# Performance work log

Hardware: AMD Instinct MI355X
Metric: run time of the kernel (lower is better)

The kernel has to match this reference:

```python
import jax, jax.numpy as jnp
import numpy as np


def setup_inputs() -> dict:
    key = jax.random.key(0)
    k1, k2 = jax.random.split(key)
    B, C, H, W, T = 64, 128, 8, 8, 100
    outputs = jax.random.normal(k1, (B, C, H, W, T), dtype=jnp.float32)
    target = jax.random.uniform(k2, (B, C, H, W, T), dtype=jnp.float32)
    return {"outputs": outputs, "target": target, "n_steps": T, "tau_s": 2}


def _psp(x, tau_s):
    # x: [B, C, H, W, T]; fixed-coefficient leaky integrator over last axis.
    # syn_t = syn_{t-1} * (1 - 1/tau_s) + x_t ; out_t = syn_t / tau_s
    decay = 1.0 - 1.0 / tau_s
    xt = jnp.moveaxis(x, -1, 0)  # [T, B, C, H, W]

    def step(syn, x_t):
        syn = syn * decay + x_t
        return syn, syn / tau_s

    syn0 = jnp.zeros(x.shape[:-1], dtype=x.dtype)
    _, syns = jax.lax.scan(step, syn0, xt)
    return jnp.moveaxis(syns, 0, -1)  # [B, C, H, W, T]


def reference(outputs, target, n_steps, tau_s):
    # n_steps is implied by the trailing axis; kept for signature fidelity.
    target_psp = _psp(target, float(tau_s))
    delta = outputs - target_psp
    return 0.5 * jnp.sum(delta * delta)
```

## Files before the change

kernel.cpp:

```cpp
#include <hip/hip_runtime.h>


constexpr int T   = 100;
constexpr int SEG = 25;
constexpr int PIX = 16;
constexpr int TF  = PIX * T;
constexpr int NCH = (TF * 4) / 1024;
constexpr int NV4 = TF / 4;

typedef const __attribute__((address_space(1))) void* gas_t;
typedef __attribute__((address_space(3))) void*       las_t;
typedef float f4 __attribute__((ext_vector_type(4)));

__global__ __launch_bounds__(64) void spike_loss_kernel(
    const float* __restrict__ tgt,
    const float* __restrict__ outs,
    const int*   __restrict__ tau_p,
    float*       __restrict__ out,
    int n_tiles, int tiles_per_block)
{
    __shared__ __align__(16) float lds_t[2][TF];

    const float tau     = (float)tau_p[0];
    const float inv_tau = 1.0f / tau;
    const float decay   = 1.0f - inv_tau;
    float d25 = 1.0f;
    #pragma unroll
    for (int i = 0; i < SEG; ++i) d25 *= decay;
    const float d50 = d25 * d25;

    const int tid = threadIdx.x;

    const int first = blockIdx.x * tiles_per_block;
    int cnt = n_tiles - first;
    if (cnt < 0) cnt = 0;
    if (cnt > tiles_per_block) cnt = tiles_per_block;
    if (cnt <= 0) return;

    float acc = 0.0f;

    auto stage = [&](int tile, int buf) {
        const float* gt = tgt + (size_t)tile * TF;
        #pragma unroll
        for (int c = 0; c < NCH; ++c) {
            __builtin_amdgcn_global_load_lds((gas_t)(gt + c * 256 + tid * 4),
                (las_t)&lds_t[buf][c * 256], 16, 0, 0);
        }
        __builtin_amdgcn_global_load_lds((gas_t)(gt + NCH * 256 + tid),
            (las_t)&lds_t[buf][NCH * 256], 4, 0, 0);
    };

    auto process = [&](int buf) {
        const int p    = tid >> 2;
        const int q    = tid & 3;
        const int base = p * T + q * SEG;

        float s[SEG];
        float syn = 0.0f;
        #pragma unroll
        for (int i = 0; i < SEG; ++i) {
            syn = fmaf(syn, decay, lds_t[buf][base + i]);
            s[i] = syn;
        }
        const float f1 = __shfl_up(syn, 1, 64);
        const float f2 = __shfl_up(syn, 2, 64);
        const float f3 = __shfl_up(syn, 3, 64);
        float carry = (q >= 1) ? f1 : 0.0f;
        if (q >= 2) carry = fmaf(f2, d25, carry);
        if (q >= 3) carry = fmaf(f3, d50, carry);

        float cp = carry;
        #pragma unroll
        for (int i = 0; i < SEG; ++i) {
            cp *= decay;
            lds_t[buf][base + i] = s[i] + cp;
        }
    };

    auto pass2 = [&](int tile, int buf) {
        const f4* o4 = (const f4*)(outs + (size_t)tile * TF);
        const f4* p4 = (const f4*)lds_t[buf];
        #pragma unroll
        for (int j = 0; j < NV4 / 64; ++j) {
            const int idx = tid + 64 * j;
            const f4 o = o4[idx];
            const f4 sy = p4[idx];
            #pragma unroll
            for (int c = 0; c < 4; ++c) {
                const float d = fmaf(sy[c], -inv_tau, o[c]);
                acc = fmaf(d, d, acc);
            }
        }
        if (tid < NV4 - (NV4 / 64) * 64) {
            const int idx = (NV4 / 64) * 64 + tid;
            const f4 o = o4[idx];
            const f4 sy = p4[idx];
            #pragma unroll
            for (int c = 0; c < 4; ++c) {
                const float d = fmaf(sy[c], -inv_tau, o[c]);
                acc = fmaf(d, d, acc);
            }
        }
    };

    stage(first, 0);

    for (int k = 0; k < cnt; ++k) {
        if (k + 1 < cnt) {
            stage(first + k + 1, (k + 1) & 1);
            asm volatile("s_waitcnt vmcnt(7)" ::: "memory");
        } else {
            asm volatile("s_waitcnt vmcnt(0)" ::: "memory");
        }
        process(k & 1);
        asm volatile("s_waitcnt lgkmcnt(0)" ::: "memory");
        pass2(first + k, k & 1);
        asm volatile("s_waitcnt lgkmcnt(0)" ::: "memory");
    }

    #pragma unroll
    for (int off = 32; off > 0; off >>= 1)
        acc += __shfl_down(acc, off, 64);
    if (tid == 0)
        atomicAdd(out, 0.5f * acc);
}

extern "C" void kernel_launch(void* const* d_in, const int* in_sizes, int n_in,
                              void* d_out, int out_size, void* d_ws, size_t ws_size,
                              hipStream_t stream) {
    const float* outs = (const float*)d_in[0];
    const float* tgt  = (const float*)d_in[1];
    const int* tau_p  = (const int*)d_in[3];
    float* out        = (float*)d_out;

    const int n_pixels = in_sizes[0] / T;
    const int n_tiles  = n_pixels / PIX;

    const int block = 64;
    const int grid  = 3072;
    const int tiles_per_block = (n_tiles + grid - 1) / grid;

    hipMemsetAsync(out, 0, sizeof(float), stream);

    spike_loss_kernel<<<grid, block, 0, stream>>>(
        tgt, outs, tau_p, out, n_tiles, tiles_per_block);
}
```

Before: 429.0 us.

## Stage outputs via LDS and fuse scan with loss, using 16-byte-aligned segments

The outputs tensor is now prefetched into LDS with async global_load_lds alongside the target, and the loss is computed in the same pass as the carry fix-up. This removes the write-back of the scanned values to LDS and the separate pass that reread them. Each pixel's time axis is split into segments of 28, 28, 28 and 16 so LDS reads can be 16-byte vectors, and the carry constants are recomputed to match. The grid is also halved so each block processes more tiles, and LDS usage doubles, which may lower occupancy.

Measured after the change: 419.2 us. 1.02x faster.

```diff
diff --git a/kernel.cpp b/kernel.cpp
--- a/kernel.cpp
+++ b/kernel.cpp
@@ -2,11 +2,9 @@
 
 
 constexpr int T   = 100;
-constexpr int SEG = 25;
 constexpr int PIX = 16;
 constexpr int TF  = PIX * T;
 constexpr int NCH = (TF * 4) / 1024;
-constexpr int NV4 = TF / 4;
 
 typedef const __attribute__((address_space(1))) void* gas_t;
 typedef __attribute__((address_space(3))) void*       las_t;
@@ -20,14 +18,15 @@
     int n_tiles, int tiles_per_block)
 {
     __shared__ __align__(16) float lds_t[2][TF];
+    __shared__ __align__(16) float lds_o[2][TF];
 
     const float tau     = (float)tau_p[0];
     const float inv_tau = 1.0f / tau;
     const float decay   = 1.0f - inv_tau;
-    float d25 = 1.0f;
+    float d28 = 1.0f;
     #pragma unroll
-    for (int i = 0; i < SEG; ++i) d25 *= decay;
-    const float d50 = d25 * d25;
+    for (int i = 0; i < 28; ++i) d28 *= decay;
+    const float d56 = d28 * d28;
 
     const int tid = threadIdx.x;
 
@@ -40,65 +39,61 @@
     float acc = 0.0f;
 
     auto stage = [&](int tile, int buf) {
-        const float* gt = tgt + (size_t)tile * TF;
+        const float* gt = tgt  + (size_t)tile * TF;
+        const float* go = outs + (size_t)tile * TF;
         #pragma unroll
         for (int c = 0; c < NCH; ++c) {
             __builtin_amdgcn_global_load_lds((gas_t)(gt + c * 256 + tid * 4),
                 (las_t)&lds_t[buf][c * 256], 16, 0, 0);
+            __builtin_amdgcn_global_load_lds((gas_t)(go + c * 256 + tid * 4),
+                (las_t)&lds_o[buf][c * 256], 16, 0, 0);
         }
         __builtin_amdgcn_global_load_lds((gas_t)(gt + NCH * 256 + tid),
             (las_t)&lds_t[buf][NCH * 256], 4, 0, 0);
+        __builtin_amdgcn_global_load_lds((gas_t)(go + NCH * 256 + tid),
+            (las_t)&lds_o[buf][NCH * 256], 4, 0, 0);
     };
 
-    auto process = [&](int buf) {
-        const int p    = tid >> 2;
-        const int q    = tid & 3;
-        const int base = p * T + q * SEG;
+    auto consume = [&](int buf) {
+        const int p  = tid >> 2;
+        const int q  = tid & 3;
+        const int fb = p * T + q * 28;
+        const f4* tb = (const f4*)&lds_t[buf][fb];
+        const f4* ob = (const f4*)&lds_o[buf][fb];
+        const int segn = (q == 3) ? 16 : 28;
 
-        float s[SEG];
+        float s[28];
         float syn = 0.0f;
         #pragma unroll
-        for (int i = 0; i < SEG; ++i) {
-            syn = fmaf(syn, decay, lds_t[buf][base + i]);
-            s[i] = syn;
+        for (int j = 0; j < 7; ++j) {
+            if (j * 4 < segn) {
+                const f4 v = tb[j];
+                #pragma unroll
+                for (int c = 0; c < 4; ++c) {
+                    syn = fmaf(syn, decay, v[c]);
+                    s[j * 4 + c] = syn;
+                }
+            }
         }
         const float f1 = __shfl_up(syn, 1, 64);
         const float f2 = __shfl_up(syn, 2, 64);
         const float f3 = __shfl_up(syn, 3, 64);
         float carry = (q >= 1) ? f1 : 0.0f;
-        if (q >= 2) carry = fmaf(f2, d25, carry);
-        if (q >= 3) carry = fmaf(f3, d50, carry);
+        if (q >= 2) carry = fmaf(f2, d28, carry);
+        if (q >= 3) carry = fmaf(f3, d56, carry);
 
         float cp = carry;
         #pragma unroll
-        for (int i = 0; i < SEG; ++i) {
-            cp *= decay;
-            lds_t[buf][base + i] = s[i] + cp;
-        }
-    };
-
-    auto pass2 = [&](int tile, int buf) {
-        const f4* o4 = (const f4*)(outs + (size_t)tile * TF);
-        const f4* p4 = (const f4*)lds_t[buf];
-        #pragma unroll
-        for (int j = 0; j < NV4 / 64; ++j) {
-            const int idx = tid + 64 * j;
-            const f4 o = o4[idx];
-            const f4 sy = p4[idx];
-            #pragma unroll
-            for (int c = 0; c < 4; ++c) {
-                const float d = fmaf(sy[c], -inv_tau, o[c]);
-                acc = fmaf(d, d, acc);
-            }
-        }
-        if (tid < NV4 - (NV4 / 64) * 64) {
-            const int idx = (NV4 / 64) * 64 + tid;
-            const f4 o = o4[idx];
-            const f4 sy = p4[idx];
-            #pragma unroll
-            for (int c = 0; c < 4; ++c) {
-                const float d = fmaf(sy[c], -inv_tau, o[c]);
-                acc = fmaf(d, d, acc);
+        for (int j = 0; j < 7; ++j) {
+            if (j * 4 < segn) {
+                const f4 ov = ob[j];
+                #pragma unroll
+                for (int c = 0; c < 4; ++c) {
+                    cp *= decay;
+                    const float st = s[j * 4 + c] + cp;
+                    const float d  = fmaf(st, -inv_tau, ov[c]);
+                    acc = fmaf(d, d, acc);
+                }
             }
         }
     };
@@ -106,15 +101,14 @@
     stage(first, 0);
 
     for (int k = 0; k < cnt; ++k) {
+        const int buf = k & 1;
         if (k + 1 < cnt) {
-            stage(first + k + 1, (k + 1) & 1);
-            asm volatile("s_waitcnt vmcnt(7)" ::: "memory");
+            stage(first + k + 1, buf ^ 1);
+            asm volatile("s_waitcnt vmcnt(14)" ::: "memory");
         } else {
             asm volatile("s_waitcnt vmcnt(0)" ::: "memory");
         }
-        process(k & 1);
-        asm volatile("s_waitcnt lgkmcnt(0)" ::: "memory");
-        pass2(first + k, k & 1);
+        consume(buf);
         asm volatile("s_waitcnt lgkmcnt(0)" ::: "memory");
     }
 
@@ -137,7 +131,7 @@
     const int n_tiles  = n_pixels / PIX;
 
     const int block = 64;
-    const int grid  = 3072;
+    const int grid  = 1536;
     const int tiles_per_block = (n_tiles + grid - 1) / grid;
 
     hipMemsetAsync(out, 0, sizeof(float), stream);
```
